# Performance work log

Hardware: AMD Instinct MI355X
Metric: run time of the kernel (lower is better)

The kernel has to match this reference:

```python
import jax, jax.numpy as jnp
import numpy as np

K = 128          # num_clusters (init kwarg k)
N_ITERS = 100    # torch loop runs up to 100 iters; converged centroids are a
                 # fixed point, so running all 100 matches the early-exit result


def _sq_dists(x, c):
    # squared Euclidean distances [N, K]; argmin identical to torch.cdist argmin
    return (jnp.sum(x * x, axis=1, keepdims=True)
            - 2.0 * (x @ c.T)
            + jnp.sum(c * c, axis=1)[None, :])


def _assign_and_update(x, c):
    ids = jnp.argmin(_sq_dists(x, c), axis=1)                     # [N]
    sums = jax.ops.segment_sum(x, ids, num_segments=K)            # [K, D]
    counts = jax.ops.segment_sum(jnp.ones((x.shape[0],), x.dtype), ids,
                                 num_segments=K)                  # [K]
    return ids, sums / counts[:, None]   # mean per cluster (NaN if empty, as in torch)


def setup_inputs() -> dict:
    key = jax.random.key(0)
    kx, kp = jax.random.split(key)
    N, D = 32768, 256
    x = jax.random.normal(kx, (N, D), dtype=jnp.float32)
    # torch.randperm(N)[:K] -> distinct initial centroid indices
    init_idx = jax.random.permutation(kp, N)[:K].astype(jnp.int32)
    return {"x": x, "init_idx": init_idx}


def reference(x, init_idx):
    c0 = x[init_idx]  # [K, D]

    def body(c, _):
        _, newc = _assign_and_update(x, c)
        return newc, None

    # 99 updates, then final assignment + update: returned ids correspond to the
    # centroids BEFORE the last update, exactly like the torch loop's last iter.
    c, _ = jax.lax.scan(body, c0, None, length=N_ITERS - 1)
    ids, c = _assign_and_update(x, c)

    logits = x @ c.T  # temperature = 1.0
    logp = jax.nn.log_softmax(logits, axis=-1)
    # CrossEntropyLoss(mean) with pseudo labels = cluster ids
    loss = -jnp.mean(jnp.take_along_axis(logp, ids[:, None], axis=1))
    return loss
```

## Files before the change

### kernel.cpp

```cpp
#include <hip/hip_runtime.h>
#include <cstdint>

#define NPTS 32768
#define DIM  256
#define NK   128
#define NITER 100
#define NBLK 256
#define NTHR 512
#define PAD  33

typedef unsigned short ushort_t;
typedef unsigned long long ull_t;
typedef __attribute__((ext_vector_type(8))) short s8v;
typedef __attribute__((ext_vector_type(4))) float f4v;

__device__ __forceinline__ unsigned short f2bf(float f) {
  unsigned u = __float_as_uint(f);
  u += 0x7fffu + ((u >> 16) & 1u);
  return (unsigned short)(u >> 16);
}
__device__ __forceinline__ float bf2f(unsigned short b) {
  return __uint_as_float(((unsigned)b) << 16);
}

__device__ __forceinline__ void cstore(float* p, float v) {
  __hip_atomic_store(p, v, __ATOMIC_RELAXED, __HIP_MEMORY_SCOPE_AGENT);
}
__device__ __forceinline__ float cload(const float* p) {
  return __hip_atomic_load(p, __ATOMIC_RELAXED, __HIP_MEMORY_SCOPE_AGENT);
}
__device__ __forceinline__ void cstorei(int* p, int v) {
  __hip_atomic_store(p, v, __ATOMIC_RELAXED, __HIP_MEMORY_SCOPE_AGENT);
}
__device__ __forceinline__ int cloadi(const int* p) {
  return __hip_atomic_load(p, __ATOMIC_RELAXED, __HIP_MEMORY_SCOPE_AGENT);
}
__device__ __forceinline__ void cstore64(ull_t* p, ull_t v) {
  __hip_atomic_store(p, v, __ATOMIC_RELAXED, __HIP_MEMORY_SCOPE_AGENT);
}
__device__ __forceinline__ ull_t cload64(const ull_t* p) {
  return __hip_atomic_load(p, __ATOMIC_RELAXED, __HIP_MEMORY_SCOPE_AGENT);
}

__device__ __forceinline__ void stage4(const ushort_t* __restrict__ src, s8v* buf, int h, int t) {
  const int lane = t & 63;
  const int wb = (t >> 6) << 6;
#pragma unroll
  for (int i = 0; i < 4; ++i) {
    const int Gb = i * 512 + wb;
    const int G  = Gb + lane;
    const int Gs = G ^ ((G >> 4) & 7);
    const char* ga = (const char*)src + (G >> 4) * 512 + h * 256 + (Gs & 15) * 16;
    __builtin_amdgcn_global_load_lds(
        (const __attribute__((address_space(1))) void*)ga,
        (__attribute__((address_space(3))) void*)((char*)buf + Gb * 16),
        16, 0, 0);
  }
}

__device__ __forceinline__ void stage_c(const ull_t* __restrict__ cpk,
                                        s8v* bh, s8v* bl, int h, int t) {
#pragma unroll
  for (int i = 0; i < 4; ++i) {
    const int G = i * NTHR + t;
    const int k = G >> 4, gcol = G & 15;
    const int sc = gcol ^ (k & 7);
    const ull_t* src = cpk + (size_t)k * 128 + h * 64 + sc * 4;
    ull_t w0 = cload64(src + 0), w1 = cload64(src + 1);
    ull_t w2 = cload64(src + 2), w3 = cload64(src + 3);
    s8v vh, vl;
    vh[0] = (short)w0; vl[0] = (short)(w0 >> 16); vh[1] = (short)(w0 >> 32); vl[1] = (short)(w0 >> 48);
    vh[2] = (short)w1; vl[2] = (short)(w1 >> 16); vh[3] = (short)(w1 >> 32); vl[3] = (short)(w1 >> 48);
    vh[4] = (short)w2; vl[4] = (short)(w2 >> 16); vh[5] = (short)(w2 >> 32); vl[5] = (short)(w2 >> 48);
    vh[6] = (short)w3; vl[6] = (short)(w3 >> 16); vh[7] = (short)(w3 >> 32); vl[7] = (short)(w3 >> 48);
    *(s8v*)((char*)bh + G * 16) = vh;
    *(s8v*)((char*)bl + G * 16) = vl;
  }
}

__device__ __forceinline__ void gbar(unsigned* flags, unsigned gen) {
  __syncthreads();
  if (threadIdx.x == 0)
    __hip_atomic_store(&flags[blockIdx.x * 16], gen, __ATOMIC_RELAXED, __HIP_MEMORY_SCOPE_AGENT);
  if (threadIdx.x < NBLK) {
    while (__hip_atomic_load(&flags[threadIdx.x * 16], __ATOMIC_RELAXED, __HIP_MEMORY_SCOPE_AGENT) < gen)
      __builtin_amdgcn_s_sleep(1);
  }
  asm volatile("" ::: "memory");
  __syncthreads();
}
__device__ __forceinline__ void gbar_pf(unsigned* flags, unsigned gen,
    const ushort_t* xhb, const ushort_t* xlb, s8v (*bufs)[2048], int t) {
  __syncthreads();
  stage4(xhb, bufs[0], 0, t);
  stage4(xlb, bufs[1], 0, t);
  if (t == 0)
    __hip_atomic_store(&flags[blockIdx.x * 16], gen, __ATOMIC_RELAXED, __HIP_MEMORY_SCOPE_AGENT);
  if (t < NBLK) {
    while (__hip_atomic_load(&flags[t * 16], __ATOMIC_RELAXED, __HIP_MEMORY_SCOPE_AGENT) < gen)
      __builtin_amdgcn_s_sleep(1);
  }
  asm volatile("" ::: "memory");
  __syncthreads();
}

struct SMa {
  s8v bufs[4][2048];
  float cns[NK];
  float redd[NK * 4];
  int   redk[NK * 4];
  float gmaxs[NK];
  float labvs[NK];
  int   labis[NK];
};

__device__ __forceinline__ void gemm_core(
    SMa& sm, int t,
    const ushort_t* __restrict__ xhb, const ushort_t* __restrict__ xlb,
    const ull_t* __restrict__ cpk, const float* __restrict__ cn, f4v (&acc)[4][2]) {
  const int lane = t & 63;
  const int w    = t >> 6;
  const int wr   = w >> 2, wc = w & 3;
  const int g    = lane >> 4, lr = lane & 15;

  if (t < NK) sm.cns[t] = cload(&cn[t]);

  const f4v zero = {0.f, 0.f, 0.f, 0.f};
#pragma unroll
  for (int i = 0; i < 4; ++i)
#pragma unroll
    for (int j = 0; j < 2; ++j) acc[i][j] = zero;

  const int swz = (lr & 7) << 4;
  int a_off[4], b_off[2];
#pragma unroll
  for (int i = 0; i < 4; ++i) a_off[i] = (wr * 64 + i * 16 + lr) * 256 + g * 16;
#pragma unroll
  for (int j = 0; j < 2; ++j) b_off[j] = (wc * 32 + j * 16 + lr) * 256 + g * 16;

  for (int h = 0; h < 2; ++h) {
    if (h == 1) {
      stage4(xhb, sm.bufs[0], 1, t);
      stage4(xlb, sm.bufs[1], 1, t);
    }
    stage_c(cpk, sm.bufs[2], sm.bufs[3], h, t);
    __syncthreads();
#pragma unroll
    for (int kk = 0; kk < 4; ++kk) {
      s8v ah[4], al[4], bh[2], bl[2];
#pragma unroll
      for (int i = 0; i < 4; ++i) {
        int o = (a_off[i] + kk * 64) ^ swz;
        ah[i] = *(const s8v*)((const char*)sm.bufs[0] + o);
        al[i] = *(const s8v*)((const char*)sm.bufs[1] + o);
      }
#pragma unroll
      for (int j = 0; j < 2; ++j) {
        int o = (b_off[j] + kk * 64) ^ swz;
        bh[j] = *(const s8v*)((const char*)sm.bufs[2] + o);
        bl[j] = *(const s8v*)((const char*)sm.bufs[3] + o);
      }
#pragma unroll
      for (int i = 0; i < 4; ++i)
#pragma unroll
        for (int j = 0; j < 2; ++j) {
          acc[i][j] = __builtin_amdgcn_mfma_f32_16x16x32_bf16(ah[i], bh[j], acc[i][j], 0, 0, 0);
          acc[i][j] = __builtin_amdgcn_mfma_f32_16x16x32_bf16(ah[i], bl[j], acc[i][j], 0, 0, 0);
          acc[i][j] = __builtin_amdgcn_mfma_f32_16x16x32_bf16(al[i], bh[j], acc[i][j], 0, 0, 0);
        }
    }
    if (h == 0) __syncthreads();
  }
}

__global__ __launch_bounds__(NTHR, 1) void kmeans_fused(
    const float* __restrict__ x, const int* __restrict__ init_idx,
    ushort_t* __restrict__ xh, ushort_t* __restrict__ xl,
    ull_t* __restrict__ cpk, float* __restrict__ cn, int* __restrict__ ids,
    float* __restrict__ psum, float* __restrict__ pcnt,
    float* __restrict__ outp, unsigned* __restrict__ flags,
    float* __restrict__ out) {
  __shared__ SMa sm;
  __shared__ float accB[NK * PAD];
  __shared__ int   idslB[1024];
  __shared__ int   cntB[NK];
  __shared__ float redsm[NTHR];
  __shared__ ushort_t hsm[DIM], lsm[DIM];
  __shared__ float cntsh;

  const int b = blockIdx.x;
  const int t = threadIdx.x;
  const int lane = t & 63;
  const int w  = t >> 6;
  const int wr = w >> 2, wc = w & 3;
  const int g  = lane >> 4, lr = lane & 15;
  const int pbase = b * 128;
  const ushort_t* xhb = xh + (size_t)pbase * DIM;
  const ushort_t* xlb = xl + (size_t)pbase * DIM;
  unsigned gen = 1;

  for (int i = 0; i < 8; ++i) {
    int gg = b * 4096 + i * NTHR + t;
    const float4* src = (const float4*)x + gg * 2;
    float4 fa = src[0], fb = src[1];
    float vv[8] = {fa.x, fa.y, fa.z, fa.w, fb.x, fb.y, fb.z, fb.w};
    s8v vh, vl;
#pragma unroll
    for (int j = 0; j < 8; ++j) {
      unsigned short hh = f2bf(vv[j]);
      vh[j] = (short)hh;
      vl[j] = (short)f2bf(vv[j] - bf2f(hh));
    }
    ((s8v*)xh)[gg] = vh;
    ((s8v*)xl)[gg] = vl;
  }

  if (b < NK) {
    float eff = 0.f;
    if (t < DIM) {
      float v = x[init_idx[b] * DIM + t];
      unsigned short hh = f2bf(v);
      unsigned short ll = f2bf(v - bf2f(hh));
      hsm[t] = hh; lsm[t] = ll;
      eff = bf2f(hh) + bf2f(ll);
    }
    __syncthreads();
    redsm[t] = eff * eff;
    if (t < NK) {
      ull_t wv = (ull_t)hsm[2 * t] | ((ull_t)lsm[2 * t] << 16)
               | ((ull_t)hsm[2 * t + 1] << 32) | ((ull_t)lsm[2 * t + 1] << 48);
      cstore64(&cpk[(size_t)b * 128 + t], wv);
    }
    __syncthreads();
    for (int s = 256; s > 0; s >>= 1) { if (t < s) redsm[t] += redsm[t + s]; __syncthreads(); }
    if (t == 0) cstore(&cn[b], redsm[0]);
  }
  gbar_pf(flags, gen, xhb, xlb, sm.bufs, t); ++gen;

  for (int it = 0; it < NITER; ++it) {
    {
      f4v acc[4][2];
      gemm_core(sm, t, xhb, xlb, cpk, cn, acc);
#pragma unroll
      for (int i = 0; i < 4; ++i) {
#pragma unroll
        for (int r = 0; r < 4; ++r) {
          int prow = wr * 64 + i * 16 + g * 4 + r;
          float bd = 1e30f; int bk = 0;
#pragma unroll
          for (int j = 0; j < 2; ++j) {
            int col = wc * 32 + j * 16 + lr;
            float s = sm.cns[col] - 2.f * acc[i][j][r];
            if (s < bd || (s == bd && col < bk)) { bd = s; bk = col; }
          }
#pragma unroll
          for (int msk = 1; msk < 16; msk <<= 1) {
            float od = __shfl_xor(bd, msk, 64);
            int   ok = __shfl_xor(bk, msk, 64);
            if (od < bd || (od == bd && ok < bk)) { bd = od; bk = ok; }
          }
          if (lr == 0) { sm.redd[prow * 4 + wc] = bd; sm.redk[prow * 4 + wc] = bk; }
        }
      }
      __syncthreads();
      if (t < NK) {
        float bd = sm.redd[t * 4]; int bk = sm.redk[t * 4];
#pragma unroll
        for (int q = 1; q < 4; ++q) {
          float dq = sm.redd[t * 4 + q]; int kq = sm.redk[t * 4 + q];
          if (dq < bd || (dq == bd && kq < bk)) { bd = dq; bk = kq; }
        }
        cstorei(&ids[pbase + t], bk);
      }
    }
    gbar(flags, gen); ++gen;

    {
      const int pg = b & 31, dg = b >> 5;
      for (int i = t; i < NK * PAD; i += NTHR) accB[i] = 0.f;
      if (t < NK) cntB[t] = 0;
      idslB[t]        = cloadi(&ids[pg * 1024 + t]);
      idslB[NTHR + t] = cloadi(&ids[pg * 1024 + NTHR + t]);
      __syncthreads();
      if (dg == 0) {
        atomicAdd(&cntB[idslB[t]], 1);
        atomicAdd(&cntB[idslB[NTHR + t]], 1);
      }
      const int qd = t & 7, ps = t >> 3;
      const float* xs = x + (size_t)pg * 1024 * DIM + dg * 32 + qd * 4;
#pragma unroll
      for (int s = 0; s < 16; ++s) {
        int pl = s * 64 + ps;
        int id = idslB[pl];
        float4 v = *(const float4*)(xs + (size_t)pl * DIM);
        atomicAdd(&accB[id * PAD + qd * 4 + 0], v.x);
        atomicAdd(&accB[id * PAD + qd * 4 + 1], v.y);
        atomicAdd(&accB[id * PAD + qd * 4 + 2], v.z);
        atomicAdd(&accB[id * PAD + qd * 4 + 3], v.w);
      }
      __syncthreads();
      const int kl = t >> 5, dl = t & 31;
#pragma unroll
      for (int s2 = 0; s2 < 8; ++s2) {
        int k2 = s2 * 16 + kl;
        cstore(&psum[(((size_t)dg * NK + k2) * 32 + pg) * 32 + dl], accB[k2 * PAD + dl]);
      }
      if (dg == 0 && t < NK)
        cstore(&pcnt[(size_t)pg * NK + t], (float)cntB[t]);
    }
    gbar(flags, gen); ++gen;

    if (b < NK) {
      const int k = b;
      const int tt = t & 255, hf = t >> 8;
      const int dgc = tt >> 5, dlc = tt & 31;
      float s = 0.f;
#pragma unroll
      for (int p2 = hf * 16; p2 < hf * 16 + 16; ++p2)
        s += cload(&psum[(((size_t)dgc * NK + k) * 32 + p2) * 32 + dlc]);
      redsm[t] = s;
      float cv = 0.f;
      if (t < 32) cv = cload(&pcnt[(size_t)t * NK + k]);
      if (t < 64) {
#pragma unroll
        for (int m = 1; m < 32; m <<= 1) cv += __shfl_xor(cv, m, 64);
      }
      if (t == 0) cntsh = cv;
      __syncthreads();
      float eff = 0.f;
      if (t < DIM) {
        float mean = (redsm[t] + redsm[t + 256]) / cntsh;
        unsigned short hh = f2bf(mean);
        unsigned short ll = f2bf(mean - bf2f(hh));
        hsm[t] = hh; lsm[t] = ll;
        eff = bf2f(hh) + bf2f(ll);
      }
      __syncthreads();
      redsm[t] = eff * eff;
      if (t < NK) {
        ull_t wv = (ull_t)hsm[2 * t] | ((ull_t)lsm[2 * t] << 16)
                 | ((ull_t)hsm[2 * t + 1] << 32) | ((ull_t)lsm[2 * t + 1] << 48);
        cstore64(&cpk[(size_t)k * 128 + t], wv);
      }
      __syncthreads();
      for (int st = 256; st > 0; st >>= 1) { if (t < st) redsm[t] += redsm[t + st]; __syncthreads(); }
      if (t == 0) cstore(&cn[k], redsm[0]);
    }
    gbar_pf(flags, gen, xhb, xlb, sm.bufs, t); ++gen;
  }

  {
    f4v acc[4][2];
    gemm_core(sm, t, xhb, xlb, cpk, cn, acc);
#pragma unroll
    for (int i = 0; i < 4; ++i) {
#pragma unroll
      for (int r = 0; r < 4; ++r) {
        int prow = wr * 64 + i * 16 + g * 4 + r;
        float m = -1e30f;
#pragma unroll
        for (int j = 0; j < 2; ++j) m = fmaxf(m, acc[i][j][r]);
#pragma unroll
        for (int msk = 1; msk < 16; msk <<= 1) m = fmaxf(m, __shfl_xor(m, msk, 64));
        if (lr == 0) sm.redd[prow * 4 + wc] = m;
      }
    }
    __syncthreads();
    if (t < NK) {
      float m = sm.redd[t * 4];
#pragma unroll
      for (int q = 1; q < 4; ++q) m = fmaxf(m, sm.redd[t * 4 + q]);
      sm.gmaxs[t] = m;
      sm.labis[t] = cloadi(&ids[pbase + t]);
    }
    __syncthreads();
#pragma unroll
    for (int i = 0; i < 4; ++i) {
#pragma unroll
      for (int r = 0; r < 4; ++r) {
        int prow = wr * 64 + i * 16 + g * 4 + r;
        float m = sm.gmaxs[prow];
        int lab = sm.labis[prow];
        float s = 0.f;
#pragma unroll
        for (int j = 0; j < 2; ++j) {
          int col = wc * 32 + j * 16 + lr;
          float v = acc[i][j][r];
          s += expf(v - m);
          if (col == lab) sm.labvs[prow] = v;
        }
#pragma unroll
        for (int msk = 1; msk < 16; msk <<= 1) s += __shfl_xor(s, msk, 64);
        if (lr == 0) sm.redd[prow * 4 + wc] = s;
      }
    }
    __syncthreads();
    if (t < NK) {
      float se = sm.redd[t * 4] + sm.redd[t * 4 + 1] + sm.redd[t * 4 + 2] + sm.redd[t * 4 + 3];
      float lse = sm.gmaxs[t] + logf(se);
      sm.gmaxs[t] = lse - sm.labvs[t];
    }
    __syncthreads();
    if (t == 0) {
      float tot = 0.f;
      for (int q = 0; q < NK; ++q) tot += sm.gmaxs[q];
      cstore(&outp[b], tot);
    }
  }
  gbar(flags, gen); ++gen;
  if (b == 0) {
    redsm[t] = (t < NBLK) ? cload(&outp[t]) : 0.f;
    __syncthreads();
    for (int s = 256; s > 0; s >>= 1) { if (t < s) redsm[t] += redsm[t + s]; __syncthreads(); }
    if (t == 0) out[0] = redsm[0] * (1.0f / (float)NPTS);
  }
}

extern "C" void kernel_launch(void* const* d_in, const int* in_sizes, int n_in,
                              void* d_out, int out_size, void* d_ws, size_t ws_size,
                              hipStream_t stream) {
  const float* x        = (const float*)d_in[0];
  const int*   init_idx = (const int*)d_in[1];
  float* out = (float*)d_out;
  char* ws = (char*)d_ws;

  ushort_t* xh  = (ushort_t*)(ws);
  ushort_t* xl  = (ushort_t*)(ws + 16777216);
  ull_t* cpk  = (ull_t*)(ws + 33554432);
  float* cn   = (float*)(ws + 33685504);
  int*   ids  = (int*)(ws + 33686016);
  float* psum = (float*)(ws + 33817088);
  float* pcnt = (float*)(ws + 38011392);
  float* outp = (float*)(ws + 38027776);
  unsigned* flags = (unsigned*)(ws + 38028800);

  hipMemsetAsync(flags, 0, 16384, stream);
  kmeans_fused<<<dim3(NBLK), dim3(NTHR), 0, stream>>>(
      x, init_idx, xh, xl, cpk, cn, ids, psum, pcnt, outp, flags, out);
}
```

Baseline: 6.976 ms.

## Double block size to 1024 threads and rework per-thread work split

Result: slower. 7.250 ms (+3.9%).

```diff
diff --git a/kernel.cpp b/kernel.cpp
--- a/kernel.cpp
+++ b/kernel.cpp
@@ -6,7 +6,7 @@
 #define NK   128
 #define NITER 100
 #define NBLK 256
-#define NTHR 512
+#define NTHR 1024
 #define PAD  33
 
 typedef unsigned short ushort_t;
@@ -46,8 +46,8 @@
   const int lane = t & 63;
   const int wb = (t >> 6) << 6;
 #pragma unroll
-  for (int i = 0; i < 4; ++i) {
-    const int Gb = i * 512 + wb;
+  for (int i = 0; i < 2; ++i) {
+    const int Gb = i * 1024 + wb;
     const int G  = Gb + lane;
     const int Gs = G ^ ((G >> 4) & 7);
     const char* ga = (const char*)src + (G >> 4) * 512 + h * 256 + (Gs & 15) * 16;
@@ -61,11 +61,11 @@
 __device__ __forceinline__ void stage_c(const ull_t* __restrict__ cpk,
                                         s8v* bh, s8v* bl, int h, int t) {
 #pragma unroll
-  for (int i = 0; i < 4; ++i) {
+  for (int i = 0; i < 2; ++i) {
     const int G = i * NTHR + t;
     const int k = G >> 4, gcol = G & 15;
-    const int sc = gcol ^ (k & 7);
-    const ull_t* src = cpk + (size_t)k * 128 + h * 64 + sc * 4;
+    const int sc2 = gcol ^ (k & 7);
+    const ull_t* src = cpk + (size_t)k * 128 + h * 64 + sc2 * 4;
     ull_t w0 = cload64(src + 0), w1 = cload64(src + 1);
     ull_t w2 = cload64(src + 2), w3 = cload64(src + 3);
     s8v vh, vl;
@@ -113,11 +113,16 @@
   float labvs[NK];
   int   labis[NK];
 };
+union ScU {
+  float accB[NK * PAD];
+  float red4[1024];
+  float redcn[1024];
+};
 
 __device__ __forceinline__ void gemm_core(
     SMa& sm, int t,
     const ushort_t* __restrict__ xhb, const ushort_t* __restrict__ xlb,
-    const ull_t* __restrict__ cpk, const float* __restrict__ cn, f4v (&acc)[4][2]) {
+    const ull_t* __restrict__ cpk, const float* __restrict__ cn, f4v (&acc)[2][2]) {
   const int lane = t & 63;
   const int w    = t >> 6;
   const int wr   = w >> 2, wc = w & 3;
@@ -127,14 +132,14 @@
 
   const f4v zero = {0.f, 0.f, 0.f, 0.f};
 #pragma unroll
-  for (int i = 0; i < 4; ++i)
+  for (int i = 0; i < 2; ++i)
 #pragma unroll
     for (int j = 0; j < 2; ++j) acc[i][j] = zero;
 
   const int swz = (lr & 7) << 4;
-  int a_off[4], b_off[2];
-#pragma unroll
-  for (int i = 0; i < 4; ++i) a_off[i] = (wr * 64 + i * 16 + lr) * 256 + g * 16;
+  int a_off[2], b_off[2];
+#pragma unroll
+  for (int i = 0; i < 2; ++i) a_off[i] = (wr * 32 + i * 16 + lr) * 256 + g * 16;
 #pragma unroll
   for (int j = 0; j < 2; ++j) b_off[j] = (wc * 32 + j * 16 + lr) * 256 + g * 16;
 
@@ -147,9 +152,9 @@
     __syncthreads();
 #pragma unroll
     for (int kk = 0; kk < 4; ++kk) {
-      s8v ah[4], al[4], bh[2], bl[2];
-#pragma unroll
-      for (int i = 0; i < 4; ++i) {
+      s8v ah[2], al[2], bh[2], bl[2];
+#pragma unroll
+      for (int i = 0; i < 2; ++i) {
         int o = (a_off[i] + kk * 64) ^ swz;
         ah[i] = *(const s8v*)((const char*)sm.bufs[0] + o);
         al[i] = *(const s8v*)((const char*)sm.bufs[1] + o);
@@ -161,7 +166,7 @@
         bl[j] = *(const s8v*)((const char*)sm.bufs[3] + o);
       }
 #pragma unroll
-      for (int i = 0; i < 4; ++i)
+      for (int i = 0; i < 2; ++i)
 #pragma unroll
         for (int j = 0; j < 2; ++j) {
           acc[i][j] = __builtin_amdgcn_mfma_f32_16x16x32_bf16(ah[i], bh[j], acc[i][j], 0, 0, 0);
@@ -181,10 +186,9 @@
     float* __restrict__ outp, unsigned* __restrict__ flags,
     float* __restrict__ out) {
   __shared__ SMa sm;
-  __shared__ float accB[NK * PAD];
-  __shared__ int   idslB[1024];
-  __shared__ int   cntB[NK];
-  __shared__ float redsm[NTHR];
+  __shared__ ScU sc;
+  __shared__ int idslB[1024];
+  __shared__ int cntB[NK];
   __shared__ ushort_t hsm[DIM], lsm[DIM];
   __shared__ float cntsh;
 
@@ -199,7 +203,7 @@
   const ushort_t* xlb = xl + (size_t)pbase * DIM;
   unsigned gen = 1;
 
-  for (int i = 0; i < 8; ++i) {
+  for (int i = 0; i < 4; ++i) {
     int gg = b * 4096 + i * NTHR + t;
     const float4* src = (const float4*)x + gg * 2;
     float4 fa = src[0], fb = src[1];
@@ -225,27 +229,27 @@
       eff = bf2f(hh) + bf2f(ll);
     }
     __syncthreads();
-    redsm[t] = eff * eff;
+    sc.redcn[t] = (t < DIM) ? eff * eff : 0.f;
     if (t < NK) {
       ull_t wv = (ull_t)hsm[2 * t] | ((ull_t)lsm[2 * t] << 16)
                | ((ull_t)hsm[2 * t + 1] << 32) | ((ull_t)lsm[2 * t + 1] << 48);
       cstore64(&cpk[(size_t)b * 128 + t], wv);
     }
     __syncthreads();
-    for (int s = 256; s > 0; s >>= 1) { if (t < s) redsm[t] += redsm[t + s]; __syncthreads(); }
-    if (t == 0) cstore(&cn[b], redsm[0]);
+    for (int s = 512; s > 0; s >>= 1) { if (t < s) sc.redcn[t] += sc.redcn[t + s]; __syncthreads(); }
+    if (t == 0) cstore(&cn[b], sc.redcn[0]);
   }
   gbar_pf(flags, gen, xhb, xlb, sm.bufs, t); ++gen;
 
   for (int it = 0; it < NITER; ++it) {
     {
-      f4v acc[4][2];
+      f4v acc[2][2];
       gemm_core(sm, t, xhb, xlb, cpk, cn, acc);
 #pragma unroll
-      for (int i = 0; i < 4; ++i) {
+      for (int i = 0; i < 2; ++i) {
 #pragma unroll
         for (int r = 0; r < 4; ++r) {
-          int prow = wr * 64 + i * 16 + g * 4 + r;
+          int prow = wr * 32 + i * 16 + g * 4 + r;
           float bd = 1e30f; int bk = 0;
 #pragma unroll
           for (int j = 0; j < 2; ++j) {
@@ -277,33 +281,36 @@
 
     {
       const int pg = b & 31, dg = b >> 5;
-      for (int i = t; i < NK * PAD; i += NTHR) accB[i] = 0.f;
+      for (int i = t; i < NK * PAD; i += NTHR) sc.accB[i] = 0.f;
       if (t < NK) cntB[t] = 0;
-      idslB[t]        = cloadi(&ids[pg * 1024 + t]);
-      idslB[NTHR + t] = cloadi(&ids[pg * 1024 + NTHR + t]);
-      __syncthreads();
-      if (dg == 0) {
-        atomicAdd(&cntB[idslB[t]], 1);
-        atomicAdd(&cntB[idslB[NTHR + t]], 1);
-      }
-      const int qd = t & 7, ps = t >> 3;
-      const float* xs = x + (size_t)pg * 1024 * DIM + dg * 32 + qd * 4;
-#pragma unroll
-      for (int s = 0; s < 16; ++s) {
-        int pl = s * 64 + ps;
-        int id = idslB[pl];
-        float4 v = *(const float4*)(xs + (size_t)pl * DIM);
-        atomicAdd(&accB[id * PAD + qd * 4 + 0], v.x);
-        atomicAdd(&accB[id * PAD + qd * 4 + 1], v.y);
-        atomicAdd(&accB[id * PAD + qd * 4 + 2], v.z);
-        atomicAdd(&accB[id * PAD + qd * 4 + 3], v.w);
-      }
-      __syncthreads();
-      const int kl = t >> 5, dl = t & 31;
-#pragma unroll
-      for (int s2 = 0; s2 < 8; ++s2) {
-        int k2 = s2 * 16 + kl;
-        cstore(&psum[(((size_t)dg * NK + k2) * 32 + pg) * 32 + dl], accB[k2 * PAD + dl]);
+      idslB[t] = cloadi(&ids[pg * 1024 + t]);
+      __syncthreads();
+      const int id = idslB[t];
+      if (dg == 0) atomicAdd(&cntB[id], 1);
+      const float* xr = x + ((size_t)pg * 1024 + t) * DIM + dg * 32;
+      f4v v0 = __builtin_nontemporal_load((const f4v*)xr + 0);
+      f4v v1 = __builtin_nontemporal_load((const f4v*)xr + 1);
+      f4v v2 = __builtin_nontemporal_load((const f4v*)xr + 2);
+      f4v v3 = __builtin_nontemporal_load((const f4v*)xr + 3);
+      f4v v4 = __builtin_nontemporal_load((const f4v*)xr + 4);
+      f4v v5 = __builtin_nontemporal_load((const f4v*)xr + 5);
+      f4v v6 = __builtin_nontemporal_load((const f4v*)xr + 6);
+      f4v v7 = __builtin_nontemporal_load((const f4v*)xr + 7);
+      float* ab = &sc.accB[id * PAD];
+      atomicAdd(ab + 0,  v0[0]); atomicAdd(ab + 1,  v0[1]); atomicAdd(ab + 2,  v0[2]); atomicAdd(ab + 3,  v0[3]);
+      atomicAdd(ab + 4,  v1[0]); atomicAdd(ab + 5,  v1[1]); atomicAdd(ab + 6,  v1[2]); atomicAdd(ab + 7,  v1[3]);
+      atomicAdd(ab + 8,  v2[0]); atomicAdd(ab + 9,  v2[1]); atomicAdd(ab + 10, v2[2]); atomicAdd(ab + 11, v2[3]);
+      atomicAdd(ab + 12, v3[0]); atomicAdd(ab + 13, v3[1]); atomicAdd(ab + 14, v3[2]); atomicAdd(ab + 15, v3[3]);
+      atomicAdd(ab + 16, v4[0]); atomicAdd(ab + 17, v4[1]); atomicAdd(ab + 18, v4[2]); atomicAdd(ab + 19, v4[3]);
+      atomicAdd(ab + 20, v5[0]); atomicAdd(ab + 21, v5[1]); atomicAdd(ab + 22, v5[2]); atomicAdd(ab + 23, v5[3]);
+      atomicAdd(ab + 24, v6[0]); atomicAdd(ab + 25, v6[1]); atomicAdd(ab + 26, v6[2]); atomicAdd(ab + 27, v6[3]);
+      atomicAdd(ab + 28, v7[0]); atomicAdd(ab + 29, v7[1]); atomicAdd(ab + 30, v7[2]); atomicAdd(ab + 31, v7[3]);
+      __syncthreads();
+#pragma unroll
+      for (int s2 = 0; s2 < 4; ++s2) {
+        int idx = s2 * NTHR + t;
+        int k2 = idx >> 5, dl = idx & 31;
+        cstore(&psum[(((size_t)dg * NK + k2) * 32 + pg) * 32 + dl], sc.accB[k2 * PAD + dl]);
       }
       if (dg == 0 && t < NK)
         cstore(&pcnt[(size_t)pg * NK + t], (float)cntB[t]);
@@ -312,15 +319,14 @@
 
     if (b < NK) {
       const int k = b;
-      const int tt = t & 255, hf = t >> 8;
+      const int hf = t >> 8, tt = t & 255;
       const int dgc = tt >> 5, dlc = tt & 31;
       float s = 0.f;
 #pragma unroll
-      for (int p2 = hf * 16; p2 < hf * 16 + 16; ++p2)
+      for (int p2 = hf * 8; p2 < hf * 8 + 8; ++p2)
         s += cload(&psum[(((size_t)dgc * NK + k) * 32 + p2) * 32 + dlc]);
-      redsm[t] = s;
-      float cv = 0.f;
-      if (t < 32) cv = cload(&pcnt[(size_t)t * NK + k]);
+      sc.red4[hf * 256 + tt] = s;
+      float cv = (t < 32) ? cload(&pcnt[(size_t)t * NK + k]) : 0.f;
       if (t < 64) {
 #pragma unroll
         for (int m = 1; m < 32; m <<= 1) cv += __shfl_xor(cv, m, 64);
@@ -329,34 +335,34 @@
       __syncthreads();
       float eff = 0.f;
       if (t < DIM) {
-        float mean = (redsm[t] + redsm[t + 256]) / cntsh;
+        float mean = (sc.red4[t] + sc.red4[256 + t] + sc.red4[512 + t] + sc.red4[768 + t]) / cntsh;
         unsigned short hh = f2bf(mean);
         unsigned short ll = f2bf(mean - bf2f(hh));
         hsm[t] = hh; lsm[t] = ll;
         eff = bf2f(hh) + bf2f(ll);
       }
       __syncthreads();
-      redsm[t] = eff * eff;
+      sc.redcn[t] = (t < DIM) ? eff * eff : 0.f;
       if (t < NK) {
         ull_t wv = (ull_t)hsm[2 * t] | ((ull_t)lsm[2 * t] << 16)
                  | ((ull_t)hsm[2 * t + 1] << 32) | ((ull_t)lsm[2 * t + 1] << 48);
         cstore64(&cpk[(size_t)k * 128 + t], wv);
       }
       __syncthreads();
-      for (int st = 256; st > 0; st >>= 1) { if (t < st) redsm[t] += redsm[t + st]; __syncthreads(); }
-      if (t == 0) cstore(&cn[k], redsm[0]);
+      for (int st = 512; st > 0; st >>= 1) { if (t < st) sc.redcn[t] += sc.redcn[t + st]; __syncthreads(); }
+      if (t == 0) cstore(&cn[k], sc.redcn[0]);
     }
     gbar_pf(flags, gen, xhb, xlb, sm.bufs, t); ++gen;
   }
 
   {
-    f4v acc[4][2];
+    f4v acc[2][2];
     gemm_core(sm, t, xhb, xlb, cpk, cn, acc);
 #pragma unroll
-    for (int i = 0; i < 4; ++i) {
+    for (int i = 0; i < 2; ++i) {
 #pragma unroll
       for (int r = 0; r < 4; ++r) {
-        int prow = wr * 64 + i * 16 + g * 4 + r;
+        int prow = wr * 32 + i * 16 + g * 4 + r;
         float m = -1e30f;
 #pragma unroll
         for (int j = 0; j < 2; ++j) m = fmaxf(m, acc[i][j][r]);
@@ -375,10 +381,10 @@
     }
     __syncthreads();
 #pragma unroll
-    for (int i = 0; i < 4; ++i) {
+    for (int i = 0; i < 2; ++i) {
 #pragma unroll
       for (int r = 0; r < 4; ++r) {
-        int prow = wr * 64 + i * 16 + g * 4 + r;
+        int prow = wr * 32 + i * 16 + g * 4 + r;
         float m = sm.gmaxs[prow];
         int lab = sm.labis[prow];
         float s = 0.f;
@@ -409,10 +415,10 @@
   }
   gbar(flags, gen); ++gen;
   if (b == 0) {
-    redsm[t] = (t < NBLK) ? cload(&outp[t]) : 0.f;
-    __syncthreads();
-    for (int s = 256; s > 0; s >>= 1) { if (t < s) redsm[t] += redsm[t + s]; __syncthreads(); }
-    if (t == 0) out[0] = redsm[0] * (1.0f / (float)NPTS);
+    sc.redcn[t] = (t < NBLK) ? cload(&outp[t]) : 0.f;
+    __syncthreads();
+    for (int s = 512; s > 0; s >>= 1) { if (t < s) sc.redcn[t] += sc.redcn[t + s]; __syncthreads(); }
+    if (t == 0) out[0] = sc.redcn[0] * (1.0f / (float)NPTS);
   }
 }
 
```
